# Kernel optimization log

Measured on AMD Instinct MI355X. Metric: run time of the kernel, lower is better.

Reference implementation:

```python
import jax, jax.numpy as jnp
import numpy as np

NUM_CLASSES = 90
NUM_LEVELS = 5
MIN_LEVEL = 3
IMAGE_SIZE = 512
NUM_SCALES = 3
ASPECT_RATIOS = (1.0, 2.0, 0.5)
ANCHOR_SCALE = 4.0
NUM_ANCHORS = NUM_SCALES * len(ASPECT_RATIOS)  # 9
MAX_DETECTION_POINTS = 5000
MAX_DETECTIONS_PER_IMAGE = 100
IOU_THRESH = 0.5
CLASS_OFFSET = 1.0e4  # > any decoded coordinate, for per-class NMS offset trick
BATCH = 16


def _make_anchor_boxes():
    """EfficientDet anchors, [N,4] as (y1,x1,y2,x2), level-major, per-cell anchors contiguous."""
    boxes_all = []
    for li in range(NUM_LEVELS):
        stride = 2 ** (MIN_LEVEL + li)
        halves = []
        for octave in range(NUM_SCALES):
            for ar in ASPECT_RATIOS:
                base = ANCHOR_SCALE * stride * 2.0 ** (octave / NUM_SCALES)
                s = np.sqrt(ar)
                halves.append((base / s / 2.0, base * s / 2.0))  # (h/2, w/2)
        halves = np.array(halves, dtype=np.float32)  # [A,2]
        c = np.arange(stride / 2.0, IMAGE_SIZE, stride, dtype=np.float32)
        yv, xv = np.meshgrid(c, c, indexing="ij")
        centers = np.stack([yv, xv], -1).reshape(-1, 1, 2)  # [H*W,1,2]
        boxes = np.concatenate([centers - halves[None], centers + halves[None]], -1)
        boxes_all.append(boxes.reshape(-1, 4))
    return np.concatenate(boxes_all, 0)


def setup_inputs() -> dict:
    key = jax.random.key(0)
    ks = jax.random.split(key, 2 * NUM_LEVELS + 1)
    inp = {}
    for li in range(NUM_LEVELS):
        hw = IMAGE_SIZE // (2 ** (MIN_LEVEL + li))
        inp[f"cls_out_{li}"] = jax.random.normal(ks[li], (BATCH, NUM_ANCHORS * NUM_CLASSES, hw, hw), jnp.float32)
        inp[f"box_out_{li}"] = jax.random.normal(ks[NUM_LEVELS + li], (BATCH, NUM_ANCHORS * 4, hw, hw), jnp.float32) * 0.1
    inp["anchor_boxes"] = jnp.asarray(_make_anchor_boxes())  # [49104,4]
    inp["image_scales"] = jax.random.uniform(ks[-1], (BATCH,), jnp.float32, 0.5, 2.0)
    return inp


def _decode(box_t, anchors):
    # box_t: [K,4] (ty,tx,th,tw); anchors: [K,4] (y1,x1,y2,x2)
    ya = (anchors[:, 0] + anchors[:, 2]) * 0.5
    xa = (anchors[:, 1] + anchors[:, 3]) * 0.5
    ha = anchors[:, 2] - anchors[:, 0]
    wa = anchors[:, 3] - anchors[:, 1]
    ty, tx, th, tw = box_t[:, 0], box_t[:, 1], box_t[:, 2], box_t[:, 3]
    h = jnp.exp(th) * ha
    w = jnp.exp(tw) * wa
    yc = ty * ha + ya
    xc = tx * wa + xa
    return jnp.stack([yc - h * 0.5, xc - w * 0.5, yc + h * 0.5, xc + w * 0.5], -1)


def _nms_single(boxes, scores, classes):
    """Per-class hard NMS via the class-offset trick; fixed 100 iterations (jit-safe)."""
    nb = boxes + classes.astype(boxes.dtype)[:, None] * CLASS_OFFSET
    area = (nb[:, 2] - nb[:, 0]) * (nb[:, 3] - nb[:, 1])

    def step(scr, _):
        i = jnp.argmax(scr)
        valid = scr[i] > -0.5  # scores are sigmoid outputs in (0,1); suppressed = -1
        b = nb[i]
        yy1 = jnp.maximum(nb[:, 0], b[0])
        xx1 = jnp.maximum(nb[:, 1], b[1])
        yy2 = jnp.minimum(nb[:, 2], b[2])
        xx2 = jnp.minimum(nb[:, 3], b[3])
        inter = jnp.clip(yy2 - yy1, 0.0) * jnp.clip(xx2 - xx1, 0.0)
        iou = inter / (area + area[i] - inter + 1e-8)
        scr = jnp.where(iou > IOU_THRESH, -1.0, scr).at[i].set(-1.0)
        return scr, (i, valid)

    _, (idx, valid) = jax.lax.scan(step, scores, None, length=MAX_DETECTIONS_PER_IMAGE)
    return idx, valid


def _forward(cls_levels, box_levels, anchor_boxes, image_scales):
    b = cls_levels[0].shape[0]
    # [B, A*C, H, W] -> [B, H*W*A, C], concat over levels
    cls_all = jnp.concatenate(
        [c.transpose(0, 2, 3, 1).reshape(b, -1, NUM_CLASSES) for c in cls_levels], 1)
    box_all = jnp.concatenate(
        [x.transpose(0, 2, 3, 1).reshape(b, -1, 4) for x in box_levels], 1)

    _, topk_idx = jax.lax.top_k(cls_all.reshape(b, -1), MAX_DETECTION_POINTS)
    indices = topk_idx // NUM_CLASSES   # anchor index  [B,K]
    classes = topk_idx % NUM_CLASSES    # class index   [B,K]

    box_topk = jnp.take_along_axis(box_all, indices[..., None], axis=1)       # [B,K,4]
    cls_topk = jnp.take_along_axis(cls_all, indices[..., None], axis=1)       # [B,K,C]
    cls_topk = jnp.take_along_axis(cls_topk, classes[..., None], axis=2)[..., 0]  # [B,K]

    def per_image(cls_i, box_i, idx_i, cls_idx_i, scale_i):
        anchors = anchor_boxes[idx_i]          # [K,4] gather
        boxes = _decode(box_i, anchors)        # [K,4]
        scores = jax.nn.sigmoid(cls_i)         # [K]
        sel, valid = _nms_single(boxes, scores, cls_idx_i)
        det = jnp.concatenate([
            boxes[sel] * scale_i,
            scores[sel][:, None],
            (cls_idx_i[sel] + 1).astype(boxes.dtype)[:, None],
        ], -1)  # [100, 6]
        return jnp.where(valid[:, None], det, 0.0)

    return jax.vmap(per_image)(cls_topk, box_topk, indices, classes, image_scales)


def reference(cls_out_0, cls_out_1, cls_out_2, cls_out_3, cls_out_4,
              box_out_0, box_out_1, box_out_2, box_out_3, box_out_4,
              anchor_boxes, image_scales):
    return _forward(
        [cls_out_0, cls_out_1, cls_out_2, cls_out_3, cls_out_4],
        [box_out_0, box_out_1, box_out_2, box_out_3, box_out_4],
        anchor_boxes, image_scales)
```

## Files before the change

kernel.cpp:

```cpp
#include <hip/hip_runtime.h>
#include <cstdint>
#include <cstddef>

#define NCLS   90
#define KSEL   5000
#define NIMG   16
#define NDET   100
#define BCAP   16384
#define QCAP   2048

__device__ inline unsigned mono(float f) {
  unsigned u = __float_as_uint(f);
  return (u & 0x80000000u) ? ~u : (u | 0x80000000u);
}
__device__ inline float inv_mono(unsigned u) {
  unsigned bits = (u & 0x80000000u) ? (u & 0x7FFFFFFFu) : ~u;
  return __uint_as_float(bits);
}
__device__ inline unsigned wave_append(bool pred, unsigned* counter) {
  unsigned long long m = __ballot(pred ? 1 : 0);
  if (m == 0ull) return 0u;
  int lane = threadIdx.x & 63;
  int lead = __ffsll((long long)m) - 1;
  unsigned base = 0;
  if (lane == lead) base = atomicAdd(counter, (unsigned)__popcll(m));
  base = __shfl(base, lead, 64);
  return base + (unsigned)__popcll(m & ((1ull << lane) - 1ull));
}

__global__ __launch_bounds__(256) void k_filter(
    const float* __restrict__ c0, const float* __restrict__ c1,
    const float* __restrict__ c2, const float* __restrict__ c3,
    const float* __restrict__ c4,
    float* __restrict__ pval, unsigned* __restrict__ pkey,
    unsigned* __restrict__ pcnt, int capp)
{
  __shared__ float    qv[QCAP];
  __shared__ unsigned qk[QCAP];
  __shared__ unsigned qn, gbase;
  int tid = threadIdx.x;
  int b = blockIdx.y;
  int bx = blockIdx.x;
  int lvl, bloc, nblk;
  if (bx < 96)       { lvl = 0; bloc = bx;       nblk = 96; }
  else if (bx < 120) { lvl = 1; bloc = bx - 96;  nblk = 24; }
  else if (bx < 126) { lvl = 2; bloc = bx - 120; nblk = 6;  }
  else if (bx < 128) { lvl = 3; bloc = bx - 126; nblk = 2;  }
  else               { lvl = 4; bloc = bx - 128; nblk = 2;  }
  const float* src; int s1, n4, posoff;
  switch (lvl) {
    case 0:  src = c0; s1 = 6; n4 = 829440; posoff = 0;     break;
    case 1:  src = c1; s1 = 5; n4 = 207360; posoff = 36864; break;
    case 2:  src = c2; s1 = 4; n4 = 51840;  posoff = 46080; break;
    case 3:  src = c3; s1 = 3; n4 = 12960;  posoff = 48384; break;
    default: src = c4; s1 = 2; n4 = 3240;   posoff = 48960; break;
  }
  src += (size_t)b * ((size_t)n4 * 4);
  if (tid == 0) qn = 0;
  __syncthreads();
  const float4* src4 = (const float4*)src;
  const unsigned msk = (1u << (2 * s1)) - 1u;
  for (int base = bloc * 512; base < n4; base += nblk * 512) {
    int iA = base + tid;
    int iB = base + 256 + tid;
    bool okA = iA < n4, okB = iB < n4;
    float4 fA, fB;
    if (okA) fA = src4[iA];
    if (okB) fB = src4[iB];
    float vs[8];
    vs[0] = fA.x; vs[1] = fA.y; vs[2] = fA.z; vs[3] = fA.w;
    vs[4] = fB.x; vs[5] = fB.y; vs[6] = fB.z; vs[7] = fB.w;
    unsigned kb[2];
    #pragma unroll
    for (int h = 0; h < 2; h++) {
      int i4 = h ? iB : iA;
      unsigned o = (unsigned)i4 << 2;
      unsigned ch  = o >> (2 * s1);
      unsigned rem = o & msk;
      unsigned a = ch / 90u;
      unsigned c = ch - a * 90u;
      unsigned y  = rem >> s1;
      unsigned x0 = rem & ((1u << s1) - 1u);
      kb[h] = ((unsigned)posoff + ((y << s1) + x0) * 9u + a) * 90u + c;
    }
    #pragma unroll
    for (int e = 0; e < 8; e++) {
      bool ok = (e < 4) ? okA : okB;
      float x = vs[e];
      unsigned key = mono(x);
      bool keep = ok && key >= 0xC0000000u;
      unsigned long long m = __ballot(keep ? 1 : 0);
      if (m) {
        int lane = tid & 63;
        int lead = __ffsll((long long)m) - 1;
        unsigned bs = 0;
        if (lane == lead) bs = atomicAdd(&qn, (unsigned)__popcll(m));
        bs = __shfl(bs, lead, 64);
        if (keep) {
          unsigned q = bs + (unsigned)__popcll(m & ((1ull << lane) - 1ull));
          if (q < QCAP) { qv[q] = x; qk[q] = kb[e >> 2] + (unsigned)(e & 3) * 810u; }
        }
      }
    }
  }
  __syncthreads();
  unsigned n = min(qn, (unsigned)QCAP);
  if (tid == 0) gbase = atomicAdd(&pcnt[b], n);
  __syncthreads();
  unsigned gb = gbase;
  for (unsigned i = tid; i < n; i += 256) {
    unsigned p = gb + i;
    if (p < (unsigned)capp) {
      pval[(size_t)b * capp + p] = qv[i];
      pkey[(size_t)b * capp + p] = qk[i];
    }
  }
}

__global__ __launch_bounds__(256) void k_hist2(
    const float* __restrict__ pval, const unsigned* __restrict__ pcnt,
    unsigned* __restrict__ ghist, int capp)
{
  __shared__ unsigned lh[1024];
  int b = blockIdx.y, ck = blockIdx.x, tid = threadIdx.x;
  for (int i = tid; i < 1024; i += 256) lh[i] = 0;
  __syncthreads();
  unsigned M = min(pcnt[b], (unsigned)capp);
  for (unsigned i = (unsigned)(ck * 256 + tid); i < M; i += 16u * 256u) {
    unsigned bkt = (mono(pval[(size_t)b * capp + i]) >> 20) - 3072u;
    atomicAdd(&lh[bkt], 1u);
  }
  __syncthreads();
  for (int i = tid; i < 1024; i += 256) {
    unsigned v = lh[i];
    if (v) atomicAdd(&ghist[b * 1024 + i], v);
  }
}

__global__ __launch_bounds__(256) void k_thresh(const unsigned* __restrict__ ghist,
                                                int* __restrict__ tinfo)
{
  int b = blockIdx.x, t = threadIdx.x;
  __shared__ unsigned h[1024];
  __shared__ unsigned csum[256];
  __shared__ unsigned basev[256];
  for (int i = t; i < 1024; i += 256) h[i] = ghist[b * 1024 + i];
  __syncthreads();
  unsigned s = 0;
  #pragma unroll
  for (int i = 0; i < 4; i++) s += h[t * 4 + i];
  csum[t] = s;
  __syncthreads();
  if (t == 0) {
    unsigned acc = 0;
    for (int i = 255; i >= 0; i--) { basev[i] = acc; acc += csum[i]; }
  }
  __syncthreads();
  unsigned run = basev[t];
  for (int j = t * 4 + 3; j >= t * 4; j--) {
    unsigned genext = run;
    run += h[j];
    if (run >= (unsigned)KSEL && genext < (unsigned)KSEL) {
      tinfo[b * 3 + 0] = j + 3072;
      tinfo[b * 3 + 1] = (int)genext;
      tinfo[b * 3 + 2] = KSEL - (int)genext;
    }
  }
}

__global__ __launch_bounds__(256) void k_classify(
    const float* __restrict__ pval, const unsigned* __restrict__ pkey,
    const unsigned* __restrict__ pcnt, const int* __restrict__ tinfo,
    float* __restrict__ aval, unsigned* __restrict__ akey, unsigned* __restrict__ acnt,
    float* __restrict__ bval, unsigned* __restrict__ bkey, unsigned* __restrict__ bcnt,
    int capp)
{
  __shared__ float    qav[1024]; __shared__ unsigned qak[1024];
  __shared__ float    qbv[1024]; __shared__ unsigned qbk[1024];
  __shared__ unsigned qan, qbn, abase, bbase;
  int b = blockIdx.y, ck = blockIdx.x, tid = threadIdx.x;
  if (tid == 0) { qan = 0; qbn = 0; }
  __syncthreads();
  unsigned M = min(pcnt[b], (unsigned)capp);
  unsigned T = (unsigned)tinfo[b * 3];
  for (unsigned i = (unsigned)(ck * 256 + tid); i < M; i += 16u * 256u) {
    float v = pval[(size_t)b * capp + i];
    unsigned fk = pkey[(size_t)b * capp + i];
    unsigned bucket = mono(v) >> 20;
    bool isab = bucket > T;
    bool isbd = bucket == T;
    unsigned pa = wave_append(isab, &qan);
    if (isab && pa < 1024u) { qav[pa] = v; qak[pa] = fk; }
    unsigned pb = wave_append(isbd, &qbn);
    if (isbd && pb < 1024u) { qbv[pb] = v; qbk[pb] = fk; }
  }
  __syncthreads();
  unsigned na = min(qan, 1024u), nb = min(qbn, 1024u);
  if (tid == 0) abase = atomicAdd(&acnt[b], na);
  if (tid == 1) bbase = atomicAdd(&bcnt[b], nb);
  __syncthreads();
  unsigned ab = abase, bb2 = bbase;
  for (unsigned i = tid; i < na; i += 256) {
    unsigned p = ab + i;
    if (p < (unsigned)KSEL) { aval[b * KSEL + p] = qav[i]; akey[b * KSEL + p] = qak[i]; }
  }
  for (unsigned i = tid; i < nb; i += 256) {
    unsigned p = bb2 + i;
    if (p < (unsigned)BCAP) { bval[b * BCAP + p] = qbv[i]; bkey[b * BCAP + p] = qbk[i]; }
  }
}

__global__ __launch_bounds__(1024) void k_boundary(
    const float* __restrict__ bval, const unsigned* __restrict__ bkey,
    const unsigned* __restrict__ bcnt, const int* __restrict__ tinfo,
    float* __restrict__ aval, unsigned* __restrict__ akey, unsigned* __restrict__ acnt)
{
  int b = blockIdx.x, tid = threadIdx.x;
  int M = min((int)bcnt[b], BCAP);
  int k = tinfo[b * 3 + 2];
  unsigned T = (unsigned)tinfo[b * 3];
  if (k <= 0) return;
  __shared__ int wred[16];
  float vv[16];
  unsigned long long cc[16];
  #pragma unroll
  for (int s = 0; s < 16; s++) {
    int i = s * 1024 + tid;
    if (i < M) {
      float v = bval[b * BCAP + i];
      unsigned fk = bkey[b * BCAP + i];
      cc[s] = ((unsigned long long)mono(v) << 32) |
              (unsigned long long)(0xFFFFFFFFu - fk);
      vv[s] = v;
    } else { cc[s] = 0ull; vv[s] = 0.f; }
  }
  unsigned long long lo = ((unsigned long long)(T << 20)) << 32;
  unsigned long long hi = (((unsigned long long)((T << 20) | 0xFFFFFu)) << 32) | 0xFFFFFFFFull;
  int w = tid >> 6, lane = tid & 63;
  while (lo < hi) {
    unsigned long long mid = lo + ((hi - lo + 1ull) >> 1);
    int c = 0;
    #pragma unroll
    for (int s = 0; s < 16; s++) c += (cc[s] >= mid) ? 1 : 0;
    for (int o = 32; o > 0; o >>= 1) c += __shfl_down(c, o, 64);
    if (lane == 0) wred[w] = c;
    __syncthreads();
    int ct = 0;
    #pragma unroll
    for (int i = 0; i < 16; i++) ct += wred[i];
    if (ct >= k) lo = mid; else hi = mid - 1ull;
    __syncthreads();
  }
  unsigned long long cstar = lo;
  #pragma unroll
  for (int s = 0; s < 16; s++) {
    bool take = cc[s] >= cstar;
    unsigned pos = wave_append(take, &acnt[b]);
    if (take && pos < (unsigned)KSEL) {
      aval[b * KSEL + pos] = vv[s];
      akey[b * KSEL + pos] = 0xFFFFFFFFu - (unsigned)(cc[s] & 0xFFFFFFFFull);
    }
  }
}

__global__ __launch_bounds__(256) void k_decode(
    const float* __restrict__ aval, const unsigned* __restrict__ akey,
    const float* __restrict__ x0p, const float* __restrict__ x1p,
    const float* __restrict__ x2p, const float* __restrict__ x3p,
    const float* __restrict__ x4p,
    const float* __restrict__ anchors,
    float* __restrict__ cand)
{
  const int N = NIMG * KSEL;
  int idx = blockIdx.x * 256 + threadIdx.x;
  if (idx >= N) return;
  int b = idx / KSEL;
  float lg = aval[idx];
  unsigned fk = akey[idx];
  unsigned pos = fk / 90u;
  unsigned c = fk - pos * 90u;
  int s1; unsigned loff; const float* bp;
  if (pos < 36864u)      { s1 = 6; loff = 0u;     bp = x0p; }
  else if (pos < 46080u) { s1 = 5; loff = 36864u; bp = x1p; }
  else if (pos < 48384u) { s1 = 4; loff = 46080u; bp = x2p; }
  else if (pos < 48960u) { s1 = 3; loff = 48384u; bp = x3p; }
  else                   { s1 = 2; loff = 48960u; bp = x4p; }
  unsigned local = pos - loff;
  unsigned cell = local / 9u;
  unsigned a = local - cell * 9u;
  unsigned hw = 1u << s1;
  unsigned hw2 = hw * hw;
  unsigned y = cell >> s1;
  unsigned x = cell & (hw - 1u);
  const float* base = bp + (size_t)b * 36u * hw2 + (size_t)(a * 4u) * hw2 + (size_t)y * hw + x;
  float ty = base[0];
  float tx = base[hw2];
  float th = base[2 * hw2];
  float tw = base[3 * hw2];
  float4 anc = ((const float4*)anchors)[pos];
  float ya = (anc.x + anc.z) * 0.5f;
  float xa = (anc.y + anc.w) * 0.5f;
  float ha = anc.z - anc.x;
  float wa = anc.w - anc.y;
  float h = expf(th) * ha;
  float w = expf(tw) * wa;
  float yc = ty * ha + ya;
  float xc = tx * wa + xa;
  cand[0 * N + idx] = yc - h * 0.5f;
  cand[1 * N + idx] = xc - w * 0.5f;
  cand[2 * N + idx] = yc + h * 0.5f;
  cand[3 * N + idx] = xc + w * 0.5f;
  cand[4 * N + idx] = lg;
  cand[5 * N + idx] = (float)c;
}

#define XCHG(JJ, UP) do {                                          \
    unsigned long long q_ = __shfl_xor(key, (JJ), 64);             \
    unsigned ps_ = __shfl_xor(sl, (JJ), 64);                       \
    bool isl_ = ((lane & (JJ)) == 0);                              \
    bool take_ = (isl_ == (UP)) ? (q_ > key) : (q_ < key);         \
    if (take_) { key = q_; sl = ps_; }                             \
  } while (0)

__global__ __launch_bounds__(1024) void k_nms(
    const float* __restrict__ cand, const unsigned* __restrict__ akey,
    const float* __restrict__ scales, float* __restrict__ out)
{
  const int N = NIMG * KSEL;
  int b = blockIdx.x, tid = threadIdx.x;
  __shared__ unsigned long long keyL[8192];
  __shared__ unsigned short slotL[8192];
  __shared__ float sy1[NDET], sx1[NDET], sy2[NDET], sx2[NDET], sar[NDET];
  __shared__ unsigned ssel[NDET];
  __shared__ int s_m;

  for (int i = tid; i < 8192; i += 1024) {
    unsigned long long key = 0ull;
    unsigned short sl = 0;
    if (i < KSEL) {
      int gi = b * KSEL + i;
      float lg = cand[4 * N + gi];
      unsigned fk = akey[gi];
      key = ((unsigned long long)mono(lg) << 32) |
            (unsigned long long)(0xFFFFFFFFu - fk);
      sl = (unsigned short)i;
    }
    keyL[i] = key; slotL[i] = sl;
  }
  __syncthreads();

  int w64 = tid >> 6, lane = tid & 63;

  for (int blk = 0; blk < 8; blk++) {
    int i = ((w64 * 8 + blk) << 6) + lane;
    unsigned long long key = keyL[i];
    unsigned sl = slotL[i];
    #pragma unroll
    for (int kk = 2; kk <= 64; kk <<= 1) {
      bool up = ((i & kk) == 0);
      #pragma unroll
      for (int jj = kk >> 1; jj >= 1; jj >>= 1) XCHG(jj, up);
    }
    keyL[i] = key; slotL[i] = (unsigned short)sl;
  }

  for (int kk = 128; kk <= 8192; kk <<= 1) {
    for (int jj = kk >> 1; jj >= 64; jj >>= 1) {
      __syncthreads();
      for (int t = tid; t < 4096; t += 1024) {
        int i = ((t & ~(jj - 1)) << 1) | (t & (jj - 1));
        int ix = i | jj;
        unsigned long long a = keyL[i], c = keyL[ix];
        bool up = ((i & kk) == 0);
        bool sw = up ? (a < c) : (a > c);
        if (sw) {
          keyL[i] = c; keyL[ix] = a;
          unsigned short st = slotL[i]; slotL[i] = slotL[ix]; slotL[ix] = st;
        }
      }
    }
    __syncthreads();
    for (int blk = 0; blk < 8; blk++) {
      int i = ((w64 * 8 + blk) << 6) + lane;
      unsigned long long key = keyL[i];
      unsigned sl = slotL[i];
      bool up = ((i & kk) == 0);
      #pragma unroll
      for (int jj = 32; jj >= 1; jj >>= 1) XCHG(jj, up);
      keyL[i] = key; slotL[i] = (unsigned short)sl;
    }
  }
  __syncthreads();

  if (tid < 64) {
    int m = 0;
    for (int base = 0; base < KSEL && m < NDET; base += 64) {
      int idx = base + lane;
      float ny1 = 0.f, nx1 = 0.f, ny2 = 0.f, nx2 = 0.f, va = 0.f;
      int slot = 0;
      bool alive = (idx < KSEL);
      if (alive) {
        slot = (int)slotL[idx];
        int gi = b * KSEL + slot;
        float y1  = cand[0 * N + gi], x1c = cand[1 * N + gi];
        float y2  = cand[2 * N + gi], x2c = cand[3 * N + gi];
        float cf  = cand[5 * N + gi];
        float off = cf * 10000.0f;
        ny1 = y1 + off; nx1 = x1c + off;
        ny2 = y2 + off; nx2 = x2c + off;
        va  = (ny2 - ny1) * (nx2 - nx1);
      }
      for (int s = 0; s < m; s++) {
        float yy1 = fmaxf(ny1, sy1[s]);
        float xx1 = fmaxf(nx1, sx1[s]);
        float yy2 = fminf(ny2, sy2[s]);
        float xx2 = fminf(nx2, sx2[s]);
        float inter = fmaxf(yy2 - yy1, 0.f) * fmaxf(xx2 - xx1, 0.f);
        float iou = inter / (va + sar[s] - inter + 1e-8f);
        if (iou > 0.5f) alive = false;
      }
      while (m < NDET) {
        unsigned long long msk = __ballot(alive ? 1 : 0);
        if (!msk) break;
        int t = __ffsll((long long)msk) - 1;
        float by1 = __shfl(ny1, t, 64);
        float bx1 = __shfl(nx1, t, 64);
        float by2 = __shfl(ny2, t, 64);
        float bx2 = __shfl(nx2, t, 64);
        float bar_ = __shfl(va, t, 64);
        int bsl = __shfl(slot, t, 64);
        if (lane == 0) {
          sy1[m] = by1; sx1[m] = bx1; sy2[m] = by2; sx2[m] = bx2; sar[m] = bar_;
          ssel[m] = (unsigned)bsl;
        }
        m++;
        if (lane == t) {
          alive = false;
        } else if (alive) {
          float yy1 = fmaxf(ny1, by1);
          float xx1 = fmaxf(nx1, bx1);
          float yy2 = fminf(ny2, by2);
          float xx2 = fminf(nx2, bx2);
          float inter = fmaxf(yy2 - yy1, 0.f) * fmaxf(xx2 - xx1, 0.f);
          float iou = inter / (va + bar_ - inter + 1e-8f);
          if (iou > 0.5f) alive = false;
        }
      }
    }
    if (lane == 0) s_m = m;
  }
  __syncthreads();

  if (tid < NDET) {
    float o[6] = {0.f, 0.f, 0.f, 0.f, 0.f, 0.f};
    if (tid < s_m) {
      int gi = b * KSEL + (int)ssel[tid];
      float s = scales[b];
      float lg = cand[4 * N + gi];
      o[0] = cand[0 * N + gi] * s;
      o[1] = cand[1 * N + gi] * s;
      o[2] = cand[2 * N + gi] * s;
      o[3] = cand[3 * N + gi] * s;
      o[4] = 1.0f / (1.0f + expf(-lg));
      o[5] = cand[5 * N + gi] + 1.0f;
    }
    float* op = out + ((size_t)b * NDET + tid) * 6;
    #pragma unroll
    for (int q = 0; q < 6; q++) op[q] = o[q];
  }
}

extern "C" void kernel_launch(void* const* d_in, const int* in_sizes, int n_in,
                              void* d_out, int out_size, void* d_ws, size_t ws_size,
                              hipStream_t stream) {
  const float* cls[5] = {nullptr, nullptr, nullptr, nullptr, nullptr};
  const float* box[5] = {nullptr, nullptr, nullptr, nullptr, nullptr};
  const float* anchors = nullptr;
  const float* scales  = nullptr;
  const long long cls_sz[5] = {53084160LL, 13271040LL, 3317760LL, 829440LL, 207360LL};
  const long long box_sz[5] = {2359296LL, 589824LL, 147456LL, 36864LL, 9216LL};
  for (int i = 0; i < n_in; i++) {
    long long s = (long long)in_sizes[i];
    const float* p = (const float*)d_in[i];
    bool m = false;
    for (int l = 0; l < 5 && !m; l++) {
      if (s == cls_sz[l]) { cls[l] = p; m = true; }
      else if (s == box_sz[l]) { box[l] = p; m = true; }
    }
    if (!m) {
      if (s == 196416LL) anchors = p;
      else if (s == 16LL) scales = p;
    }
  }
  for (int l = 0; l < 5; l++) if (!cls[l] || !box[l]) return;
  if (!anchors || !scales) return;

  char* w = (char*)d_ws;
  unsigned* ghist = (unsigned*)(w);
  unsigned* pcnt  = (unsigned*)(w + 65536);
  unsigned* acnt  = (unsigned*)(w + 65600);
  unsigned* bcnt  = (unsigned*)(w + 65664);
  int*      tinfo = (int*)(w + 65728);
  size_t off = 66048;
  size_t fixed_rest = (size_t)NIMG * KSEL * 4 * 2
                    + (size_t)NIMG * BCAP * 4 * 2
                    + (size_t)6 * NIMG * KSEL * 4;
  long long avail = (long long)ws_size - (long long)off - (long long)fixed_rest;
  int capp = 131072;
  long long maxcap = avail / (NIMG * 8);
  if (maxcap < (long long)capp) capp = (int)(maxcap > 1 ? maxcap : 1);

  float*    pval = (float*)(w + off);    off += (size_t)NIMG * capp * 4;
  unsigned* pkey = (unsigned*)(w + off); off += (size_t)NIMG * capp * 4;
  float*    aval = (float*)(w + off);    off += (size_t)NIMG * KSEL * 4;
  unsigned* akey = (unsigned*)(w + off); off += (size_t)NIMG * KSEL * 4;
  float*    bval = (float*)(w + off);    off += (size_t)NIMG * BCAP * 4;
  unsigned* bkey = (unsigned*)(w + off); off += (size_t)NIMG * BCAP * 4;
  float*    cand = (float*)(w + off);    off += (size_t)6 * NIMG * KSEL * 4;

  hipMemsetAsync(d_ws, 0, 66048, stream);

  k_filter<<<dim3(130, NIMG), 256, 0, stream>>>(cls[0], cls[1], cls[2], cls[3], cls[4],
                                                pval, pkey, pcnt, capp);
  k_hist2<<<dim3(16, NIMG), 256, 0, stream>>>(pval, pcnt, ghist, capp);
  k_thresh<<<NIMG, 256, 0, stream>>>(ghist, tinfo);
  k_classify<<<dim3(16, NIMG), 256, 0, stream>>>(pval, pkey, pcnt, tinfo,
                                                 aval, akey, acnt, bval, bkey, bcnt, capp);
  k_boundary<<<NIMG, 1024, 0, stream>>>(bval, bkey, bcnt, tinfo, aval, akey, acnt);
  k_decode<<<(NIMG * KSEL + 255) / 256, 256, 0, stream>>>(
      aval, akey, box[0], box[1], box[2], box[3], box[4], anchors, cand);
  k_nms<<<NIMG, 1024, 0, stream>>>(cand, akey, scales, (float*)d_out);
}
```

Baseline: 608.8 us.

## Replace full bitonic sort in NMS with histogram-selected partial rank sort

The NMS kernel now builds a 1024-bin histogram on the top bits of the score keys to find a threshold admitting at least 512 candidates. Only those candidates are compacted and ranked by counting, and greedy NMS runs on that subset. It falls back to the original 8192-element bitonic sort if the subset is too large or yields fewer than 100 detections. Separately, the filter kernel batches its eight per-element ballots into one shared atomic per wave. The aim is to cut sort and barrier cost per image, at the price of a possible double pass when the fallback triggers.

```diff
diff --git a/kernel.cpp b/kernel.cpp
--- a/kernel.cpp
+++ b/kernel.cpp
@@ -39,6 +39,7 @@
   __shared__ unsigned qk[QCAP];
   __shared__ unsigned qn, gbase;
   int tid = threadIdx.x;
+  int lane = tid & 63;
   int b = blockIdx.y;
   int bx = blockIdx.x;
   int lvl, bloc, nblk;
@@ -60,6 +61,7 @@
   __syncthreads();
   const float4* src4 = (const float4*)src;
   const unsigned msk = (1u << (2 * s1)) - 1u;
+  const unsigned long long ltm = (1ull << lane) - 1ull;
   for (int base = bloc * 512; base < n4; base += nblk * 512) {
     int iA = base + tid;
     int iB = base + 256 + tid;
@@ -83,22 +85,25 @@
       unsigned x0 = rem & ((1u << s1) - 1u);
       kb[h] = ((unsigned)posoff + ((y << s1) + x0) * 9u + a) * 90u + c;
     }
+    unsigned long long mm[8];
     #pragma unroll
     for (int e = 0; e < 8; e++) {
       bool ok = (e < 4) ? okA : okB;
-      float x = vs[e];
-      unsigned key = mono(x);
-      bool keep = ok && key >= 0xC0000000u;
-      unsigned long long m = __ballot(keep ? 1 : 0);
-      if (m) {
-        int lane = tid & 63;
-        int lead = __ffsll((long long)m) - 1;
-        unsigned bs = 0;
-        if (lane == lead) bs = atomicAdd(&qn, (unsigned)__popcll(m));
-        bs = __shfl(bs, lead, 64);
-        if (keep) {
-          unsigned q = bs + (unsigned)__popcll(m & ((1ull << lane) - 1ull));
-          if (q < QCAP) { qv[q] = x; qk[q] = kb[e >> 2] + (unsigned)(e & 3) * 810u; }
+      unsigned key = mono(vs[e]);
+      mm[e] = __ballot((ok && key >= 0xC0000000u) ? 1 : 0);
+    }
+    unsigned pre[8], run = 0;
+    #pragma unroll
+    for (int e = 0; e < 8; e++) { pre[e] = run; run += (unsigned)__popcll(mm[e]); }
+    if (run) {
+      unsigned bs = 0;
+      if (lane == 0) bs = atomicAdd(&qn, run);
+      bs = __shfl(bs, 0, 64);
+      #pragma unroll
+      for (int e = 0; e < 8; e++) {
+        if ((mm[e] >> lane) & 1ull) {
+          unsigned q = bs + pre[e] + (unsigned)__popcll(mm[e] & ltm);
+          if (q < QCAP) { qv[q] = vs[e]; qk[q] = kb[e >> 2] + (unsigned)(e & 3) * 810u; }
         }
       }
     }
@@ -314,6 +319,70 @@
   cand[5 * N + idx] = (float)c;
 }
 
+__device__ inline int greedy_run(const float* __restrict__ cand, int b,
+                                 const unsigned short* __restrict__ order, int count,
+                                 float* sy1, float* sx1, float* sy2, float* sx2,
+                                 float* sar, unsigned* ssel)
+{
+  const int N = NIMG * KSEL;
+  int lane = threadIdx.x & 63;
+  int m = 0;
+  for (int base = 0; base < count && m < NDET; base += 64) {
+    int idx = base + lane;
+    float ny1 = 0.f, nx1 = 0.f, ny2 = 0.f, nx2 = 0.f, va = 0.f;
+    int slot = 0;
+    bool alive = (idx < count);
+    if (alive) {
+      slot = (int)order[idx];
+      int gi = b * KSEL + slot;
+      float y1  = cand[0 * N + gi], x1c = cand[1 * N + gi];
+      float y2  = cand[2 * N + gi], x2c = cand[3 * N + gi];
+      float cf  = cand[5 * N + gi];
+      float off = cf * 10000.0f;
+      ny1 = y1 + off; nx1 = x1c + off;
+      ny2 = y2 + off; nx2 = x2c + off;
+      va  = (ny2 - ny1) * (nx2 - nx1);
+    }
+    for (int s = 0; s < m; s++) {
+      float yy1 = fmaxf(ny1, sy1[s]);
+      float xx1 = fmaxf(nx1, sx1[s]);
+      float yy2 = fminf(ny2, sy2[s]);
+      float xx2 = fminf(nx2, sx2[s]);
+      float inter = fmaxf(yy2 - yy1, 0.f) * fmaxf(xx2 - xx1, 0.f);
+      float iou = inter / (va + sar[s] - inter + 1e-8f);
+      if (iou > 0.5f) alive = false;
+    }
+    while (m < NDET) {
+      unsigned long long msk = __ballot(alive ? 1 : 0);
+      if (!msk) break;
+      int t = __ffsll((long long)msk) - 1;
+      float by1 = __shfl(ny1, t, 64);
+      float bx1 = __shfl(nx1, t, 64);
+      float by2 = __shfl(ny2, t, 64);
+      float bx2 = __shfl(nx2, t, 64);
+      float bar_ = __shfl(va, t, 64);
+      int bsl = __shfl(slot, t, 64);
+      if (lane == 0) {
+        sy1[m] = by1; sx1[m] = bx1; sy2[m] = by2; sx2[m] = bx2; sar[m] = bar_;
+        ssel[m] = (unsigned)bsl;
+      }
+      m++;
+      if (lane == t) {
+        alive = false;
+      } else if (alive) {
+        float yy1 = fmaxf(ny1, by1);
+        float xx1 = fmaxf(nx1, bx1);
+        float yy2 = fminf(ny2, by2);
+        float xx2 = fminf(nx2, bx2);
+        float inter = fmaxf(yy2 - yy1, 0.f) * fmaxf(xx2 - xx1, 0.f);
+        float iou = inter / (va + bar_ - inter + 1e-8f);
+        if (iou > 0.5f) alive = false;
+      }
+    }
+  }
+  return m;
+}
+
 #define XCHG(JJ, UP) do {                                          \
     unsigned long long q_ = __shfl_xor(key, (JJ), 64);             \
     unsigned ps_ = __shfl_xor(sl, (JJ), 64);                       \
@@ -330,124 +399,154 @@
   int b = blockIdx.x, tid = threadIdx.x;
   __shared__ unsigned long long keyL[8192];
   __shared__ unsigned short slotL[8192];
+  __shared__ unsigned csum[256], basev[256];
   __shared__ float sy1[NDET], sx1[NDET], sy2[NDET], sx2[NDET], sar[NDET];
   __shared__ unsigned ssel[NDET];
-  __shared__ int s_m;
-
-  for (int i = tid; i < 8192; i += 1024) {
-    unsigned long long key = 0ull;
-    unsigned short sl = 0;
-    if (i < KSEL) {
-      int gi = b * KSEL + i;
+  __shared__ int s_m, s_T2, s_M2;
+  __shared__ unsigned s_cn;
+
+  int w64 = tid >> 6, lane = tid & 63;
+
+  unsigned*           hist  = (unsigned*)keyL;
+  unsigned*           ge    = ((unsigned*)keyL) + 1024;
+  unsigned long long* keyC  = keyL + 1024;
+  unsigned short*     slotC = slotL;
+  unsigned short*     sortedSlot = slotL + 2048;
+
+  hist[tid] = 0;
+  if (tid == 0) { s_cn = 0; s_T2 = 0; s_M2 = 0x7FFFFFFF; }
+  __syncthreads();
+
+  unsigned long long cc[5];
+  #pragma unroll
+  for (int k = 0; k < 5; k++) {
+    int j = tid + k * 1024;
+    if (j < KSEL) {
+      int gi = b * KSEL + j;
       float lg = cand[4 * N + gi];
       unsigned fk = akey[gi];
-      key = ((unsigned long long)mono(lg) << 32) |
-            (unsigned long long)(0xFFFFFFFFu - fk);
-      sl = (unsigned short)i;
-    }
-    keyL[i] = key; slotL[i] = sl;
-  }
-  __syncthreads();
-
-  int w64 = tid >> 6, lane = tid & 63;
-
-  for (int blk = 0; blk < 8; blk++) {
-    int i = ((w64 * 8 + blk) << 6) + lane;
-    unsigned long long key = keyL[i];
-    unsigned sl = slotL[i];
+      cc[k] = ((unsigned long long)mono(lg) << 32) |
+              (unsigned long long)(0xFFFFFFFFu - fk);
+      atomicAdd(&hist[((unsigned)(cc[k] >> 52) - 3072u) & 1023u], 1u);
+    } else cc[k] = 0ull;
+  }
+  __syncthreads();
+
+  if (tid < 256) {
+    csum[tid] = hist[tid * 4] + hist[tid * 4 + 1] + hist[tid * 4 + 2] + hist[tid * 4 + 3];
+  }
+  __syncthreads();
+  if (tid == 0) {
+    unsigned acc = 0;
+    for (int i = 255; i >= 0; i--) { basev[i] = acc; acc += csum[i]; }
+  }
+  __syncthreads();
+  if (tid < 256) {
+    unsigned run = basev[tid];
+    for (int j = tid * 4 + 3; j >= tid * 4; j--) { run += hist[j]; ge[j] = run; }
+  }
+  __syncthreads();
+  {
+    unsigned g = ge[tid];
+    unsigned gn = (tid == 1023) ? 0u : ge[tid + 1];
+    if (g >= 512u && gn < 512u) { s_T2 = tid; s_M2 = (int)g; }
+  }
+  __syncthreads();
+  int T2 = s_T2, M2 = s_M2;
+  bool need_full = (M2 > 2048);
+
+  if (!need_full) {
     #pragma unroll
-    for (int kk = 2; kk <= 64; kk <<= 1) {
-      bool up = ((i & kk) == 0);
-      #pragma unroll
-      for (int jj = kk >> 1; jj >= 1; jj >>= 1) XCHG(jj, up);
-    }
-    keyL[i] = key; slotL[i] = (unsigned short)sl;
-  }
-
-  for (int kk = 128; kk <= 8192; kk <<= 1) {
-    for (int jj = kk >> 1; jj >= 64; jj >>= 1) {
-      __syncthreads();
-      for (int t = tid; t < 4096; t += 1024) {
-        int i = ((t & ~(jj - 1)) << 1) | (t & (jj - 1));
-        int ix = i | jj;
-        unsigned long long a = keyL[i], c = keyL[ix];
-        bool up = ((i & kk) == 0);
-        bool sw = up ? (a < c) : (a > c);
-        if (sw) {
-          keyL[i] = c; keyL[ix] = a;
-          unsigned short st = slotL[i]; slotL[i] = slotL[ix]; slotL[ix] = st;
-        }
-      }
-    }
-    __syncthreads();
+    for (int k = 0; k < 5; k++) {
+      int j = tid + k * 1024;
+      bool p = (j < KSEL) && ((int)((unsigned)(cc[k] >> 52) - 3072u) >= T2);
+      unsigned pos = wave_append(p, &s_cn);
+      if (p && pos < 2048u) { keyC[pos] = cc[k]; slotC[pos] = (unsigned short)j; }
+    }
+    __syncthreads();
+    for (int j = tid; j < M2; j += 1024) {
+      unsigned long long kj = keyC[j];
+      int r = 0, i = 0;
+      for (; i + 4 <= M2; i += 4) {
+        r += (keyC[i]     > kj) ? 1 : 0;
+        r += (keyC[i + 1] > kj) ? 1 : 0;
+        r += (keyC[i + 2] > kj) ? 1 : 0;
+        r += (keyC[i + 3] > kj) ? 1 : 0;
+      }
+      for (; i < M2; i++) r += (keyC[i] > kj) ? 1 : 0;
+      if (r < 2048) sortedSlot[r] = slotC[j];
+    }
+    __syncthreads();
+    if (tid < 64) {
+      int m = greedy_run(cand, b, sortedSlot, M2, sy1, sx1, sy2, sx2, sar, ssel);
+      if (lane == 0) s_m = m;
+    }
+    __syncthreads();
+    if (s_m < NDET) need_full = true;
+  }
+
+  if (need_full) {
+    __syncthreads();
+    for (int i = tid; i < 8192; i += 1024) {
+      unsigned long long key = 0ull;
+      unsigned short sl = 0;
+      if (i < KSEL) {
+        int gi = b * KSEL + i;
+        float lg = cand[4 * N + gi];
+        unsigned fk = akey[gi];
+        key = ((unsigned long long)mono(lg) << 32) |
+              (unsigned long long)(0xFFFFFFFFu - fk);
+        sl = (unsigned short)i;
+      }
+      keyL[i] = key; slotL[i] = sl;
+    }
+    __syncthreads();
+
     for (int blk = 0; blk < 8; blk++) {
       int i = ((w64 * 8 + blk) << 6) + lane;
       unsigned long long key = keyL[i];
       unsigned sl = slotL[i];
-      bool up = ((i & kk) == 0);
       #pragma unroll
-      for (int jj = 32; jj >= 1; jj >>= 1) XCHG(jj, up);
+      for (int kk = 2; kk <= 64; kk <<= 1) {
+        bool up = ((i & kk) == 0);
+        #pragma unroll
+        for (int jj = kk >> 1; jj >= 1; jj >>= 1) XCHG(jj, up);
+      }
       keyL[i] = key; slotL[i] = (unsigned short)sl;
     }
-  }
-  __syncthreads();
-
-  if (tid < 64) {
-    int m = 0;
-    for (int base = 0; base < KSEL && m < NDET; base += 64) {
-      int idx = base + lane;
-      float ny1 = 0.f, nx1 = 0.f, ny2 = 0.f, nx2 = 0.f, va = 0.f;
-      int slot = 0;
-      bool alive = (idx < KSEL);
-      if (alive) {
-        slot = (int)slotL[idx];
-        int gi = b * KSEL + slot;
-        float y1  = cand[0 * N + gi], x1c = cand[1 * N + gi];
-        float y2  = cand[2 * N + gi], x2c = cand[3 * N + gi];
-        float cf  = cand[5 * N + gi];
-        float off = cf * 10000.0f;
-        ny1 = y1 + off; nx1 = x1c + off;
-        ny2 = y2 + off; nx2 = x2c + off;
-        va  = (ny2 - ny1) * (nx2 - nx1);
-      }
-      for (int s = 0; s < m; s++) {
-        float yy1 = fmaxf(ny1, sy1[s]);
-        float xx1 = fmaxf(nx1, sx1[s]);
-        float yy2 = fminf(ny2, sy2[s]);
-        float xx2 = fminf(nx2, sx2[s]);
-        float inter = fmaxf(yy2 - yy1, 0.f) * fmaxf(xx2 - xx1, 0.f);
-        float iou = inter / (va + sar[s] - inter + 1e-8f);
-        if (iou > 0.5f) alive = false;
-      }
-      while (m < NDET) {
-        unsigned long long msk = __ballot(alive ? 1 : 0);
-        if (!msk) break;
-        int t = __ffsll((long long)msk) - 1;
-        float by1 = __shfl(ny1, t, 64);
-        float bx1 = __shfl(nx1, t, 64);
-        float by2 = __shfl(ny2, t, 64);
-        float bx2 = __shfl(nx2, t, 64);
-        float bar_ = __shfl(va, t, 64);
-        int bsl = __shfl(slot, t, 64);
-        if (lane == 0) {
-          sy1[m] = by1; sx1[m] = bx1; sy2[m] = by2; sx2[m] = bx2; sar[m] = bar_;
-          ssel[m] = (unsigned)bsl;
+
+    for (int kk = 128; kk <= 8192; kk <<= 1) {
+      for (int jj = kk >> 1; jj >= 64; jj >>= 1) {
+        __syncthreads();
+        for (int t = tid; t < 4096; t += 1024) {
+          int i = ((t & ~(jj - 1)) << 1) | (t & (jj - 1));
+          int ix = i | jj;
+          unsigned long long a = keyL[i], c = keyL[ix];
+          bool up = ((i & kk) == 0);
+          bool sw = up ? (a < c) : (a > c);
+          if (sw) {
+            keyL[i] = c; keyL[ix] = a;
+            unsigned short st = slotL[i]; slotL[i] = slotL[ix]; slotL[ix] = st;
+          }
         }
-        m++;
-        if (lane == t) {
-          alive = false;
-        } else if (alive) {
-          float yy1 = fmaxf(ny1, by1);
-          float xx1 = fmaxf(nx1, bx1);
-          float yy2 = fminf(ny2, by2);
-          float xx2 = fminf(nx2, bx2);
-          float inter = fmaxf(yy2 - yy1, 0.f) * fmaxf(xx2 - xx1, 0.f);
-          float iou = inter / (va + bar_ - inter + 1e-8f);
-          if (iou > 0.5f) alive = false;
-        }
-      }
-    }
-    if (lane == 0) s_m = m;
+      }
+      __syncthreads();
+      for (int blk = 0; blk < 8; blk++) {
+        int i = ((w64 * 8 + blk) << 6) + lane;
+        unsigned long long key = keyL[i];
+        unsigned sl = slotL[i];
+        bool up = ((i & kk) == 0);
+        #pragma unroll
+        for (int jj = 32; jj >= 1; jj >>= 1) XCHG(jj, up);
+        keyL[i] = key; slotL[i] = (unsigned short)sl;
+      }
+    }
+    __syncthreads();
+
+    if (tid < 64) {
+      int m = greedy_run(cand, b, slotL, KSEL, sy1, sx1, sy2, sx2, sar, ssel);
+      if (lane == 0) s_m = m;
+    }
   }
   __syncthreads();
 
```

New measurement: 549.2 us. 1.11x faster.
